# Performance work log

Measured on AMD Instinct MI355X. Metric: run time of the kernel, lower is better.

## Reference

```python
import jax, jax.numpy as jnp
import numpy as np

B, H, N, D, R, HIDDEN = 4, 12, 1025, 64, 1, 32


def _make_tables(N, R):
    # Geometry tables, mirroring FlexAttentionCPB.init_tables
    P = N - R
    S = int(P ** 0.5)
    assert S * S == P
    rng = np.arange(-(S - 1), S, dtype=np.float32)        # [2S-1]
    dY, dX = np.meshgrid(rng, rng, indexing='ij')
    rel = np.stack([dY / max(S - 1, 1), dX / max(S - 1, 1)], axis=-1).reshape(-1, 2)
    rel_table = np.sign(rel) * np.log1p(np.abs(rel))      # [(2S-1)^2, 2]
    yy = np.arange(S)
    Y, X = np.meshgrid(yy, yy, indexing='ij')
    flat = np.stack([Y, X], 0).reshape(2, -1)             # [2, P]
    d = (flat[:, :, None] - flat[:, None, :]).transpose(1, 2, 0).copy()  # [P,P,2]
    d[:, :, 0] += S - 1
    d[:, :, 1] += S - 1
    d[:, :, 0] *= 2 * S - 1
    l_idx = d.sum(-1).astype(np.int32)
    idx = np.full((N, N), -1, dtype=np.int32)
    idx[R:, R:] = l_idx
    return jnp.asarray(rel_table, jnp.float32), jnp.asarray(idx)


def setup_inputs() -> dict:
    key = jax.random.key(0)
    ks = jax.random.split(key, 8)
    rel_table, idx_table = _make_tables(N, R)
    return {
        'q': jax.random.normal(ks[0], (B, H, N, D), jnp.float32),
        'k': jax.random.normal(ks[1], (B, H, N, D), jnp.float32),
        'v': jax.random.normal(ks[2], (B, H, N, D), jnp.float32),
        'mu': jax.random.normal(ks[3], (B, H, 2, N), jnp.float32),
        'w1': jax.random.normal(ks[4], (2, HIDDEN), jnp.float32) * 0.5,
        'b1': jax.random.normal(ks[5], (HIDDEN,), jnp.float32) * 0.05,
        'w2': jax.random.normal(ks[6], (HIDDEN, H), jnp.float32) * 0.1,
        'gamma': jnp.zeros((H,), jnp.float32),   # nn.Parameter(torch.zeros(H))
        'rel_table': rel_table,
        'idx_table': idx_table,
    }


def reference(q, k, v, mu, w1, b1, w2, gamma, rel_table, idx_table):
    d = q.shape[-1]
    # CPB MLP: Linear(2,hidden)+GELU(exact)+Linear(hidden,H,no bias) -> [L,H]
    bt = jax.nn.gelu(rel_table @ w1 + b1, approximate=False) @ w2
    has_bias = (idx_table >= 0)                       # [N,N] == (q>=R)&(kv>=R)
    idx_c = jnp.where(has_bias, idx_table, 0)
    bias = jnp.transpose(bt[idx_c], (2, 0, 1))        # [H,N,N]
    mu_q = mu[:, :, 0, :]                             # [B,H,N]
    mu_k = mu[:, :, 1, :]
    gate = jax.nn.sigmoid(gamma)[None, :, None, None] * (
        mu_q[..., :, None] + mu_k[..., None, :])      # [B,H,N,N]
    scale = 1.0 / jnp.sqrt(jnp.asarray(d, q.dtype))
    scores = jnp.einsum('bhqd,bhkd->bhqk', q, k) * scale
    scores = scores + has_bias[None, None].astype(scores.dtype) * gate * bias[None]
    attn = jax.nn.softmax(scores, axis=-1)
    return jnp.einsum('bhqk,bhkd->bhqd', attn, v)
```

## Files before the change

kernel.cpp:

```cpp
#include <hip/hip_runtime.h>
#include <math.h>

#define B_ 4
#define H_ 12
#define N_ 1025
#define D_ 64
#define HID_ 32
#define TBL_ 3969
#define NQT 17
#define NBLK (B_ * H_ * NQT)
#define LOG2E 1.44269504f
#define THR_ 12.0f

typedef _Float16 half8 __attribute__((ext_vector_type(8)));
typedef __fp16 fp16x2 __attribute__((ext_vector_type(2)));
typedef float f32x4 __attribute__((ext_vector_type(4)));

#if defined(__has_builtin)
#if __has_builtin(__builtin_amdgcn_exp2f)
#define EX2 __builtin_amdgcn_exp2f
#else
#define EX2 exp2f
#endif
#else
#define EX2 exp2f
#endif

#define BTT_OFF 0
#define AKT_OFF 190512
#define KF_OFF 399408
#define VF_OFF 7084080

__device__ __forceinline__ void stage16(const _Float16* gsrc, _Float16* ldst) {
    __builtin_amdgcn_global_load_lds(
        (const __attribute__((address_space(1))) void*)gsrc,
        (__attribute__((address_space(3))) void*)ldst, 16, 0, 0);
}

__global__ __launch_bounds__(256) void prep(
    const float* __restrict__ K, const float* __restrict__ V,
    const float* __restrict__ MU, const float* __restrict__ GAMMA,
    const float* __restrict__ rel, const float* __restrict__ w1,
    const float* __restrict__ b1, const float* __restrict__ w2,
    _Float16* __restrict__ Kf, _Float16* __restrict__ Vf,
    float* __restrict__ akT, float* __restrict__ btT) {
    const int bid = blockIdx.x;
    const int tid = threadIdx.x;
    if (bid < NBLK) {
        __shared__ float Vls[64 * 65];
        const int bh = bid / NQT, kt = bid % NQT;
        const size_t base = (size_t)bh * (N_ * D_);
        const int k0 = kt * 64;
#pragma unroll
        for (int it = 0; it < 4; ++it) {
            const int idx = it * 256 + tid;
            const int kr = idx >> 4, c4 = (idx & 15) << 2;
            const int kg = k0 + kr;
            float4 v4 = make_float4(0, 0, 0, 0);
            if (kg < N_) v4 = *(const float4*)(V + base + (size_t)kg * D_ + c4);
            Vls[(c4 + 0) * 65 + kr] = v4.x;
            Vls[(c4 + 1) * 65 + kr] = v4.y;
            Vls[(c4 + 2) * 65 + kr] = v4.z;
            Vls[(c4 + 3) * 65 + kr] = v4.w;
        }
        __syncthreads();
        const int lane = tid & 63, lq = lane & 15, g = lane >> 4;
        const int fbh = tid >> 6;
        const size_t tb = (size_t)(bh * NQT + kt) * 4096;
#pragma unroll
        for (int x = 0; x < 2; ++x) {
            const int fb = fbh + x * 4;
            {
                const int kh = fb >> 2, dg = fb & 3;
                const float* vp = &Vls[(dg * 16 + lq) * 65 + kh * 32 + g * 8];
                half8 v8;
#pragma unroll
                for (int j = 0; j < 8; ++j) v8[j] = (_Float16)vp[j];
                *(half8*)&Vf[tb + fb * 512 + lane * 8] = v8;
            }
            {
                const int row = k0 + (fb >> 1) * 16 + lq;
                const int col = (fb & 1) * 32 + g * 8;
                half8 k8;
                if (row < N_) {
                    const float4* p = (const float4*)(K + base + (size_t)row * D_ + col);
                    float4 a = p[0], b = p[1];
                    k8[0] = (_Float16)a.x; k8[1] = (_Float16)a.y;
                    k8[2] = (_Float16)a.z; k8[3] = (_Float16)a.w;
                    k8[4] = (_Float16)b.x; k8[5] = (_Float16)b.y;
                    k8[6] = (_Float16)b.z; k8[7] = (_Float16)b.w;
                } else {
#pragma unroll
                    for (int j = 0; j < 8; ++j) k8[j] = (_Float16)0.f;
                }
                *(half8*)&Kf[tb + fb * 512 + lane * 8] = k8;
            }
        }
        if (tid < 64) {
            const int kk = k0 + tid;
            const int h = bh % H_;
            const float sgl = LOG2E / (1.f + __expf(-GAMMA[h]));
            float a = 0.f;
            if (kk >= 1 && kk < N_) a = sgl * MU[((size_t)bh * 2 + 1) * N_ + kk];
            akT[bh * 1088 + kk] = a;
        }
    } else {
        const int i = (bid - NBLK) * 256 + tid;
        if (i < TBL_) {
            const float x0 = rel[2 * i + 0], x1 = rel[2 * i + 1];
            float acc[H_];
#pragma unroll
            for (int h = 0; h < H_; ++h) acc[h] = 0.f;
#pragma unroll
            for (int j = 0; j < HID_; ++j) {
                float t = fmaf(x0, w1[j], fmaf(x1, w1[HID_ + j], b1[j]));
                float gl = 0.5f * t * (1.f + erff(t * 0.7071067811865475f));
#pragma unroll
                for (int h = 0; h < H_; ++h) acc[h] = fmaf(gl, w2[j * H_ + h], acc[h]);
            }
#pragma unroll
            for (int h = 0; h < H_; ++h) btT[h * TBL_ + i] = acc[h];
        }
    }
}

__global__ __launch_bounds__(256, 4) void flex_attn(
    const float* __restrict__ Q, const _Float16* __restrict__ Kf,
    const _Float16* __restrict__ Vf, const float* __restrict__ MU,
    const float* __restrict__ GAMMA, const char* __restrict__ btb,
    const float* __restrict__ akT, float* __restrict__ OUT) {
    __shared__ __align__(16) _Float16 Ks[2][4096];
    __shared__ __align__(16) _Float16 Vs[2][4096];
    __shared__ __align__(16) _Float16 Pl[4][1024];

    const int bid = blockIdx.x;
    const int swz0 = (bid & 7) * (NBLK / 8) + (bid >> 3);
    const int bh = swz0 / NQT;
    const int qt = swz0 % NQT;
    const int h = bh % H_;
    const int tid = threadIdx.x;
    const int w = tid >> 6;
    const int lane = tid & 63;
    const int lq = lane & 15;
    const int g = lane >> 4;

    const size_t base = (size_t)bh * (N_ * D_);
    const float sg = LOG2E / (1.f + __expf(-GAMMA[h]));

    const int qrow = qt * 64 + w * 16 + lq;
    const bool qv = qrow < N_;

    half8 qf[2];
#pragma unroll
    for (int dh = 0; dh < 2; ++dh) {
        float4 t0 = make_float4(0, 0, 0, 0), t1 = t0;
        if (qv) {
            const float4* qp = (const float4*)(Q + base + (size_t)qrow * D_ + dh * 32 + g * 8);
            t0 = qp[0]; t1 = qp[1];
        }
        const float qs = 0.125f * LOG2E;
        half8 q8;
        q8[0] = (_Float16)(t0.x * qs); q8[1] = (_Float16)(t0.y * qs);
        q8[2] = (_Float16)(t0.z * qs); q8[3] = (_Float16)(t0.w * qs);
        q8[4] = (_Float16)(t1.x * qs); q8[5] = (_Float16)(t1.y * qs);
        q8[6] = (_Float16)(t1.z * qs); q8[7] = (_Float16)(t1.w * qs);
        qf[dh] = q8;
    }

    const bool qb = qv && (qrow >= 1);
    const float qbf = qb ? 1.f : 0.f;
    float aq = 0.f;
    int cq = 0;
    if (qb) {
        const int pq = qrow - 1;
        cq = (pq >> 5) * 63 + (pq & 31);
        aq = sg * MU[(size_t)bh * 2 * N_ + qrow];
    }
    int boffs[16];
#pragma unroll
    for (int kg = 0; kg < 4; ++kg) {
#pragma unroll
        for (int r = 0; r < 4; ++r) {
            const int pk = kg * 16 + g * 4 + r - 1;
            const int ck = (pk >> 5) * 63 + (pk & 31);
            boffs[kg * 4 + r] = (h * TBL_ + cq + 1984 - ck) * 4 + 2048;
        }
    }
    const float* akb = akT + bh * 1088;
    const _Float16* kfb = Kf + (size_t)bh * NQT * 4096;
    const _Float16* vfb = Vf + (size_t)bh * NQT * 4096;

    f32x4 o[4];
    const f32x4 zz = {0.f, 0.f, 0.f, 0.f};
#pragma unroll
    for (int dg = 0; dg < 4; ++dg) o[dg] = zz;
    float m = 0.f, lsum = 0.f;

    stage16(kfb + (2 * w + 0) * 512 + lane * 8, &Ks[0][(2 * w + 0) * 512]);
    stage16(kfb + (2 * w + 1) * 512 + lane * 8, &Ks[0][(2 * w + 1) * 512]);
    stage16(vfb + (2 * w + 0) * 512 + lane * 8, &Vs[0][(2 * w + 0) * 512]);
    stage16(vfb + (2 * w + 1) * 512 + lane * 8, &Vs[0][(2 * w + 1) * 512]);
    __syncthreads();

    const int pswz = (lq & 7) << 4;
    char* plw = (char*)&Pl[w][0];

    for (int t = 0; t < NQT; ++t) {
        const int buf = t & 1;
        const int kt0 = t * 64;

        float bt16[16];
#pragma unroll
        for (int i = 0; i < 16; ++i) {
            int off = boffs[i];
            off = off < 2048 ? 2048 : off;
            bt16[i] = *(const float*)(btb + (uint32_t)off);
            boffs[i] -= 504;
        }
        f32x4 akq[4];
#pragma unroll
        for (int kg = 0; kg < 4; ++kg)
            akq[kg] = *(const f32x4*)(akb + kt0 + kg * 16 + g * 4);

        if (t + 1 < NQT) {
            const _Float16* kn = kfb + (size_t)(t + 1) * 4096;
            const _Float16* vn = vfb + (size_t)(t + 1) * 4096;
            stage16(kn + (2 * w + 0) * 512 + lane * 8, &Ks[buf ^ 1][(2 * w + 0) * 512]);
            stage16(kn + (2 * w + 1) * 512 + lane * 8, &Ks[buf ^ 1][(2 * w + 1) * 512]);
            stage16(vn + (2 * w + 0) * 512 + lane * 8, &Vs[buf ^ 1][(2 * w + 0) * 512]);
            stage16(vn + (2 * w + 1) * 512 + lane * 8, &Vs[buf ^ 1][(2 * w + 1) * 512]);
        }

        const _Float16* ksl = &Ks[buf][lane * 8];
        f32x4 sa[4];
#pragma unroll
        for (int kg = 0; kg < 4; ++kg) {
            half8 a0 = *(const half8*)(ksl + (2 * kg + 0) * 512);
            half8 a1 = *(const half8*)(ksl + (2 * kg + 1) * 512);
            f32x4 z = zz;
            z = __builtin_amdgcn_mfma_f32_16x16x32_f16(a0, qf[0], z, 0, 0, 0);
            z = __builtin_amdgcn_mfma_f32_16x16x32_f16(a1, qf[1], z, 0, 0, 0);
            sa[kg] = z;
        }

        if (t == 0 && g == 0) bt16[0] = 0.f;
        float s[16];
#pragma unroll
        for (int kg = 0; kg < 4; ++kg) {
#pragma unroll
            for (int r = 0; r < 4; ++r) {
                const int i = kg * 4 + r;
                s[i] = fmaf(fmaf(qbf, akq[kg][r], aq), bt16[i], sa[kg][r]);
            }
        }
        if (t == NQT - 1) {
#pragma unroll
            for (int kg = 0; kg < 4; ++kg)
#pragma unroll
                for (int r = 0; r < 4; ++r) {
                    const int i = kg * 4 + r;
                    if (1024 + kg * 16 + g * 4 + r >= N_) s[i] = -1e30f;
                }
        }

        float lmax = s[0];
#pragma unroll
        for (int i = 1; i < 16; ++i) lmax = fmaxf(lmax, s[i]);
        if (t == 0) {
            float mt = fmaxf(lmax, __shfl_xor(lmax, 16));
            m = fmaxf(mt, __shfl_xor(mt, 32));
        } else if (!__all(lmax <= m + THR_)) {
            float mt = fmaxf(lmax, __shfl_xor(lmax, 16));
            mt = fmaxf(mt, __shfl_xor(mt, 32));
            const float mnew = fmaxf(m, mt);
            const float cc = EX2(m - mnew);
            m = mnew;
            lsum *= cc;
            float cc4[4];
#pragma unroll
            for (int r = 0; r < 4; ++r) cc4[r] = __shfl(cc, g * 4 + r);
#pragma unroll
            for (int dg = 0; dg < 4; ++dg)
#pragma unroll
                for (int r = 0; r < 4; ++r) o[dg][r] *= cc4[r];
        }
        float pv16[16];
        float ls0 = 0.f, ls1 = 0.f;
#pragma unroll
        for (int i = 0; i < 16; i += 2) {
            pv16[i] = EX2(s[i] - m);
            pv16[i + 1] = EX2(s[i + 1] - m);
            ls0 += pv16[i];
            ls1 += pv16[i + 1];
        }
        lsum += ls0 + ls1;

#pragma unroll
        for (int kg = 0; kg < 4; ++kg) {
            fp16x2 h0 = __builtin_amdgcn_cvt_pkrtz(pv16[kg * 4 + 0], pv16[kg * 4 + 1]);
            fp16x2 h1 = __builtin_amdgcn_cvt_pkrtz(pv16[kg * 4 + 2], pv16[kg * 4 + 3]);
            uint2 u = make_uint2(__builtin_bit_cast(uint32_t, h0),
                                 __builtin_bit_cast(uint32_t, h1));
            *(uint2*)(plw + lq * 128 + ((kg * 32 + g * 8) ^ pswz)) = u;
        }

#pragma unroll
        for (int kh = 0; kh < 2; ++kh) {
            half8 pa = *(const half8*)(plw + lq * 128 + ((kh * 64 + g * 16) ^ pswz));
#pragma unroll
            for (int dg = 0; dg < 4; ++dg) {
                half8 vb8 = *(const half8*)&Vs[buf][(kh * 4 + dg) * 512 + lane * 8];
                o[dg] = __builtin_amdgcn_mfma_f32_16x16x32_f16(pa, vb8, o[dg], 0, 0, 0);
            }
        }
        __syncthreads();
    }

    lsum += __shfl_xor(lsum, 16);
    lsum += __shfl_xor(lsum, 32);
    const float linv = 1.f / lsum;
    float li4[4];
#pragma unroll
    for (int r = 0; r < 4; ++r) li4[r] = __shfl(linv, g * 4 + r);
#pragma unroll
    for (int dg = 0; dg < 4; ++dg) {
#pragma unroll
        for (int r = 0; r < 4; ++r) {
            const int qq = qt * 64 + w * 16 + g * 4 + r;
            if (qq < N_) OUT[base + (size_t)qq * D_ + dg * 16 + lq] = o[dg][r] * li4[r];
        }
    }
}

extern "C" void kernel_launch(void* const* d_in, const int* in_sizes, int n_in,
                              void* d_out, int out_size, void* d_ws, size_t ws_size,
                              hipStream_t stream) {
    const float* q = (const float*)d_in[0];
    const float* k = (const float*)d_in[1];
    const float* v = (const float*)d_in[2];
    const float* mu = (const float*)d_in[3];
    const float* w1 = (const float*)d_in[4];
    const float* b1 = (const float*)d_in[5];
    const float* w2 = (const float*)d_in[6];
    const float* gamma = (const float*)d_in[7];
    const float* rel = (const float*)d_in[8];

    char* ws = (char*)d_ws;
    float* btT = (float*)(ws + BTT_OFF);
    float* akT = (float*)(ws + AKT_OFF);
    _Float16* Kf = (_Float16*)(ws + KF_OFF);
    _Float16* Vf = (_Float16*)(ws + VF_OFF);

    prep<<<NBLK + (TBL_ + 255) / 256, 256, 0, stream>>>(k, v, mu, gamma, rel, w1, b1, w2,
                                                        Kf, Vf, akT, btT);
    flex_attn<<<NBLK, 256, 0, stream>>>(q, Kf, Vf, mu, gamma, ws - 2048, akT, (float*)d_out);
}
```

Before: 65.81 us.

## Switch attention to 32x32x16 MFMA with split-KV waves and register P

```diff
diff --git a/kernel.cpp b/kernel.cpp
--- a/kernel.cpp
+++ b/kernel.cpp
@@ -15,6 +15,7 @@
 typedef _Float16 half8 __attribute__((ext_vector_type(8)));
 typedef __fp16 fp16x2 __attribute__((ext_vector_type(2)));
 typedef float f32x4 __attribute__((ext_vector_type(4)));
+typedef float f32x16 __attribute__((ext_vector_type(16)));
 
 #if defined(__has_builtin)
 #if __has_builtin(__builtin_amdgcn_exp2f)
@@ -35,6 +36,11 @@
     __builtin_amdgcn_global_load_lds(
         (const __attribute__((address_space(1))) void*)gsrc,
         (__attribute__((address_space(3))) void*)ldst, 16, 0, 0);
+}
+
+__device__ __forceinline__ uint32_t pk2(float a, float b) {
+    fp16x2 t = __builtin_amdgcn_cvt_pkrtz(a, b);
+    return __builtin_bit_cast(uint32_t, t);
 }
 
 __global__ __launch_bounds__(256) void prep(
@@ -47,53 +53,59 @@
     const int bid = blockIdx.x;
     const int tid = threadIdx.x;
     if (bid < NBLK) {
-        __shared__ float Vls[64 * 65];
+        __shared__ uint32_t VlsU[64 * 36];
         const int bh = bid / NQT, kt = bid % NQT;
         const size_t base = (size_t)bh * (N_ * D_);
         const int k0 = kt * 64;
-#pragma unroll
-        for (int it = 0; it < 4; ++it) {
-            const int idx = it * 256 + tid;
-            const int kr = idx >> 4, c4 = (idx & 15) << 2;
-            const int kg = k0 + kr;
-            float4 v4 = make_float4(0, 0, 0, 0);
-            if (kg < N_) v4 = *(const float4*)(V + base + (size_t)kg * D_ + c4);
-            Vls[(c4 + 0) * 65 + kr] = v4.x;
-            Vls[(c4 + 1) * 65 + kr] = v4.y;
-            Vls[(c4 + 2) * 65 + kr] = v4.z;
-            Vls[(c4 + 3) * 65 + kr] = v4.w;
-        }
-        __syncthreads();
-        const int lane = tid & 63, lq = lane & 15, g = lane >> 4;
+        const int lane = tid & 63, q5 = lane & 31, hi = lane >> 5;
         const int fbh = tid >> 6;
         const size_t tb = (size_t)(bh * NQT + kt) * 4096;
+        float4 kld[2][2];
 #pragma unroll
         for (int x = 0; x < 2; ++x) {
-            const int fb = fbh + x * 4;
+            const int fk = fbh + 4 * x;
+            const int wk = fk >> 2, dc = fk & 3;
+            const int row = k0 + wk * 32 + q5;
+            const int col = dc * 16 + hi * 8;
+            kld[x][0] = make_float4(0, 0, 0, 0);
+            kld[x][1] = kld[x][0];
+            if (row < N_) {
+                const float4* p = (const float4*)(K + base + (size_t)row * D_ + col);
+                kld[x][0] = p[0];
+                kld[x][1] = p[1];
+            }
+        }
+#pragma unroll
+        for (int it = 0; it < 2; ++it) {
+            const int idx = it * 256 + tid;
+            const int p = idx >> 4;
+            const int c4 = (idx & 15) << 2;
+            const int r0 = k0 + 2 * p;
+            float4 a = make_float4(0, 0, 0, 0), b = a;
+            if (r0 < N_) a = *(const float4*)(V + base + (size_t)r0 * D_ + c4);
+            if (r0 + 1 < N_) b = *(const float4*)(V + base + (size_t)(r0 + 1) * D_ + c4);
+            VlsU[(c4 + 0) * 36 + p] = pk2(a.x, b.x);
+            VlsU[(c4 + 1) * 36 + p] = pk2(a.y, b.y);
+            VlsU[(c4 + 2) * 36 + p] = pk2(a.z, b.z);
+            VlsU[(c4 + 3) * 36 + p] = pk2(a.w, b.w);
+        }
+        __syncthreads();
+#pragma unroll
+        for (int x = 0; x < 2; ++x) {
+            const int f = fbh + 4 * x;
             {
-                const int kh = fb >> 2, dg = fb & 3;
-                const float* vp = &Vls[(dg * 16 + lq) * 65 + kh * 32 + g * 8];
-                half8 v8;
-#pragma unroll
-                for (int j = 0; j < 8; ++j) v8[j] = (_Float16)vp[j];
-                *(half8*)&Vf[tb + fb * 512 + lane * 8] = v8;
+                const int kc = f >> 1, dh = f & 1;
+                uint4 u = *(const uint4*)&VlsU[(dh * 32 + q5) * 36 + kc * 8 + hi * 4];
+                *(uint4*)&Vf[tb + f * 512 + lane * 8] = u;
             }
             {
-                const int row = k0 + (fb >> 1) * 16 + lq;
-                const int col = (fb & 1) * 32 + g * 8;
                 half8 k8;
-                if (row < N_) {
-                    const float4* p = (const float4*)(K + base + (size_t)row * D_ + col);
-                    float4 a = p[0], b = p[1];
-                    k8[0] = (_Float16)a.x; k8[1] = (_Float16)a.y;
-                    k8[2] = (_Float16)a.z; k8[3] = (_Float16)a.w;
-                    k8[4] = (_Float16)b.x; k8[5] = (_Float16)b.y;
-                    k8[6] = (_Float16)b.z; k8[7] = (_Float16)b.w;
-                } else {
-#pragma unroll
-                    for (int j = 0; j < 8; ++j) k8[j] = (_Float16)0.f;
-                }
-                *(half8*)&Kf[tb + fb * 512 + lane * 8] = k8;
+                float4 a = kld[x][0], b = kld[x][1];
+                k8[0] = (_Float16)a.x; k8[1] = (_Float16)a.y;
+                k8[2] = (_Float16)a.z; k8[3] = (_Float16)a.w;
+                k8[4] = (_Float16)b.x; k8[5] = (_Float16)b.y;
+                k8[6] = (_Float16)b.z; k8[7] = (_Float16)b.w;
+                *(half8*)&Kf[tb + f * 512 + lane * 8] = k8;
             }
         }
         if (tid < 64) {
@@ -124,14 +136,13 @@
     }
 }
 
-__global__ __launch_bounds__(256, 4) void flex_attn(
+__global__ __launch_bounds__(256, 3) void flex_attn(
     const float* __restrict__ Q, const _Float16* __restrict__ Kf,
     const _Float16* __restrict__ Vf, const float* __restrict__ MU,
     const float* __restrict__ GAMMA, const char* __restrict__ btb,
     const float* __restrict__ akT, float* __restrict__ OUT) {
     __shared__ __align__(16) _Float16 Ks[2][4096];
     __shared__ __align__(16) _Float16 Vs[2][4096];
-    __shared__ __align__(16) _Float16 Pl[4][1024];
 
     const int bid = blockIdx.x;
     const int swz0 = (bid & 7) * (NBLK / 8) + (bid >> 3);
@@ -140,31 +151,33 @@
     const int h = bh % H_;
     const int tid = threadIdx.x;
     const int w = tid >> 6;
+    const int wk = w & 1;
+    const int wq = w >> 1;
     const int lane = tid & 63;
-    const int lq = lane & 15;
-    const int g = lane >> 4;
+    const int q5 = lane & 31;
+    const int hi = lane >> 5;
 
     const size_t base = (size_t)bh * (N_ * D_);
     const float sg = LOG2E / (1.f + __expf(-GAMMA[h]));
 
-    const int qrow = qt * 64 + w * 16 + lq;
+    const int qrow = qt * 64 + wq * 32 + q5;
     const bool qv = qrow < N_;
 
-    half8 qf[2];
-#pragma unroll
-    for (int dh = 0; dh < 2; ++dh) {
+    half8 qf[4];
+    const float qs = 0.125f * LOG2E;
+#pragma unroll
+    for (int dc = 0; dc < 4; ++dc) {
         float4 t0 = make_float4(0, 0, 0, 0), t1 = t0;
         if (qv) {
-            const float4* qp = (const float4*)(Q + base + (size_t)qrow * D_ + dh * 32 + g * 8);
+            const float4* qp = (const float4*)(Q + base + (size_t)qrow * D_ + dc * 16 + hi * 8);
             t0 = qp[0]; t1 = qp[1];
         }
-        const float qs = 0.125f * LOG2E;
         half8 q8;
         q8[0] = (_Float16)(t0.x * qs); q8[1] = (_Float16)(t0.y * qs);
         q8[2] = (_Float16)(t0.z * qs); q8[3] = (_Float16)(t0.w * qs);
         q8[4] = (_Float16)(t1.x * qs); q8[5] = (_Float16)(t1.y * qs);
         q8[6] = (_Float16)(t1.z * qs); q8[7] = (_Float16)(t1.w * qs);
-        qf[dh] = q8;
+        qf[dc] = q8;
     }
 
     const bool qb = qv && (qrow >= 1);
@@ -178,23 +191,19 @@
     }
     int boffs[16];
 #pragma unroll
-    for (int kg = 0; kg < 4; ++kg) {
-#pragma unroll
-        for (int r = 0; r < 4; ++r) {
-            const int pk = kg * 16 + g * 4 + r - 1;
-            const int ck = (pk >> 5) * 63 + (pk & 31);
-            boffs[kg * 4 + r] = (h * TBL_ + cq + 1984 - ck) * 4 + 2048;
-        }
+    for (int r = 0; r < 16; ++r) {
+        const int pk = wk * 32 + (r & 3) + 8 * (r >> 2) + 4 * hi - 1;
+        const int ck = (pk >> 5) * 63 + (pk & 31);
+        boffs[r] = (h * TBL_ + cq + 1984 - ck) * 4 + 2048;
     }
     const float* akb = akT + bh * 1088;
     const _Float16* kfb = Kf + (size_t)bh * NQT * 4096;
     const _Float16* vfb = Vf + (size_t)bh * NQT * 4096;
 
-    f32x4 o[4];
-    const f32x4 zz = {0.f, 0.f, 0.f, 0.f};
-#pragma unroll
-    for (int dg = 0; dg < 4; ++dg) o[dg] = zz;
-    float m = 0.f, lsum = 0.f;
+    f32x16 oA, oB;
+#pragma unroll
+    for (int r = 0; r < 16; ++r) { oA[r] = 0.f; oB[r] = 0.f; }
+    float m = 0.f, l = 0.f;
 
     stage16(kfb + (2 * w + 0) * 512 + lane * 8, &Ks[0][(2 * w + 0) * 512]);
     stage16(kfb + (2 * w + 1) * 512 + lane * 8, &Ks[0][(2 * w + 1) * 512]);
@@ -202,25 +211,23 @@
     stage16(vfb + (2 * w + 1) * 512 + lane * 8, &Vs[0][(2 * w + 1) * 512]);
     __syncthreads();
 
-    const int pswz = (lq & 7) << 4;
-    char* plw = (char*)&Pl[w][0];
-
+#pragma unroll 1
     for (int t = 0; t < NQT; ++t) {
         const int buf = t & 1;
         const int kt0 = t * 64;
 
         float bt16[16];
 #pragma unroll
-        for (int i = 0; i < 16; ++i) {
-            int off = boffs[i];
+        for (int r = 0; r < 16; ++r) {
+            int off = boffs[r];
             off = off < 2048 ? 2048 : off;
-            bt16[i] = *(const float*)(btb + (uint32_t)off);
-            boffs[i] -= 504;
+            bt16[r] = *(const float*)(btb + (uint32_t)off);
+            boffs[r] -= 504;
         }
         f32x4 akq[4];
 #pragma unroll
-        for (int kg = 0; kg < 4; ++kg)
-            akq[kg] = *(const f32x4*)(akb + kt0 + kg * 16 + g * 4);
+        for (int mi = 0; mi < 4; ++mi)
+            akq[mi] = *(const f32x4*)(akb + kt0 + wk * 32 + 8 * mi + 4 * hi);
 
         if (t + 1 < NQT) {
             const _Float16* kn = kfb + (size_t)(t + 1) * 4096;
@@ -231,103 +238,122 @@
             stage16(vn + (2 * w + 1) * 512 + lane * 8, &Vs[buf ^ 1][(2 * w + 1) * 512]);
         }
 
-        const _Float16* ksl = &Ks[buf][lane * 8];
-        f32x4 sa[4];
-#pragma unroll
-        for (int kg = 0; kg < 4; ++kg) {
-            half8 a0 = *(const half8*)(ksl + (2 * kg + 0) * 512);
-            half8 a1 = *(const half8*)(ksl + (2 * kg + 1) * 512);
-            f32x4 z = zz;
-            z = __builtin_amdgcn_mfma_f32_16x16x32_f16(a0, qf[0], z, 0, 0, 0);
-            z = __builtin_amdgcn_mfma_f32_16x16x32_f16(a1, qf[1], z, 0, 0, 0);
-            sa[kg] = z;
-        }
-
-        if (t == 0 && g == 0) bt16[0] = 0.f;
+        const _Float16* ksl = &Ks[buf][wk * 2048 + lane * 8];
+        f32x16 sa;
+#pragma unroll
+        for (int r = 0; r < 16; ++r) sa[r] = 0.f;
+#pragma unroll
+        for (int dc = 0; dc < 4; ++dc) {
+            half8 a = *(const half8*)(ksl + dc * 512);
+            sa = __builtin_amdgcn_mfma_f32_32x32x16_f16(a, qf[dc], sa, 0, 0, 0);
+        }
+
+        if (t == 0 && wk == 0) bt16[0] = hi ? bt16[0] : 0.f;
         float s[16];
 #pragma unroll
-        for (int kg = 0; kg < 4; ++kg) {
-#pragma unroll
-            for (int r = 0; r < 4; ++r) {
-                const int i = kg * 4 + r;
-                s[i] = fmaf(fmaf(qbf, akq[kg][r], aq), bt16[i], sa[kg][r]);
-            }
-        }
+        for (int r = 0; r < 16; ++r)
+            s[r] = fmaf(fmaf(qbf, akq[r >> 2][r & 3], aq), bt16[r], sa[r]);
         if (t == NQT - 1) {
 #pragma unroll
-            for (int kg = 0; kg < 4; ++kg)
-#pragma unroll
-                for (int r = 0; r < 4; ++r) {
-                    const int i = kg * 4 + r;
-                    if (1024 + kg * 16 + g * 4 + r >= N_) s[i] = -1e30f;
-                }
-        }
-
-        float lmax = s[0];
-#pragma unroll
-        for (int i = 1; i < 16; ++i) lmax = fmaxf(lmax, s[i]);
+            for (int r = 0; r < 16; ++r) {
+                const bool keep = (wk == 0) && (r == 0) && (hi == 0);
+                s[r] = keep ? s[r] : -1e30f;
+            }
+        }
+
+        float mt = s[0];
+#pragma unroll
+        for (int r = 1; r < 16; ++r) mt = fmaxf(mt, s[r]);
         if (t == 0) {
-            float mt = fmaxf(lmax, __shfl_xor(lmax, 16));
             m = fmaxf(mt, __shfl_xor(mt, 32));
-        } else if (!__all(lmax <= m + THR_)) {
-            float mt = fmaxf(lmax, __shfl_xor(lmax, 16));
-            mt = fmaxf(mt, __shfl_xor(mt, 32));
-            const float mnew = fmaxf(m, mt);
+        } else if (!__all(mt <= m + THR_)) {
+            const float mp = fmaxf(mt, __shfl_xor(mt, 32));
+            const float mnew = fmaxf(m, mp);
             const float cc = EX2(m - mnew);
             m = mnew;
-            lsum *= cc;
-            float cc4[4];
-#pragma unroll
-            for (int r = 0; r < 4; ++r) cc4[r] = __shfl(cc, g * 4 + r);
-#pragma unroll
-            for (int dg = 0; dg < 4; ++dg)
-#pragma unroll
-                for (int r = 0; r < 4; ++r) o[dg][r] *= cc4[r];
+            l *= cc;
+#pragma unroll
+            for (int r = 0; r < 16; ++r) {
+                const int qr = (r & 3) + 8 * (r >> 2) + 4 * hi;
+                const float ccr = __shfl(cc, qr);
+                oA[r] *= ccr;
+                oB[r] *= ccr;
+            }
         }
         float pv16[16];
         float ls0 = 0.f, ls1 = 0.f;
 #pragma unroll
-        for (int i = 0; i < 16; i += 2) {
-            pv16[i] = EX2(s[i] - m);
-            pv16[i + 1] = EX2(s[i + 1] - m);
-            ls0 += pv16[i];
-            ls1 += pv16[i + 1];
-        }
-        lsum += ls0 + ls1;
-
-#pragma unroll
-        for (int kg = 0; kg < 4; ++kg) {
-            fp16x2 h0 = __builtin_amdgcn_cvt_pkrtz(pv16[kg * 4 + 0], pv16[kg * 4 + 1]);
-            fp16x2 h1 = __builtin_amdgcn_cvt_pkrtz(pv16[kg * 4 + 2], pv16[kg * 4 + 3]);
-            uint2 u = make_uint2(__builtin_bit_cast(uint32_t, h0),
-                                 __builtin_bit_cast(uint32_t, h1));
-            *(uint2*)(plw + lq * 128 + ((kg * 32 + g * 8) ^ pswz)) = u;
-        }
-
-#pragma unroll
-        for (int kh = 0; kh < 2; ++kh) {
-            half8 pa = *(const half8*)(plw + lq * 128 + ((kh * 64 + g * 16) ^ pswz));
-#pragma unroll
-            for (int dg = 0; dg < 4; ++dg) {
-                half8 vb8 = *(const half8*)&Vs[buf][(kh * 4 + dg) * 512 + lane * 8];
-                o[dg] = __builtin_amdgcn_mfma_f32_16x16x32_f16(pa, vb8, o[dg], 0, 0, 0);
-            }
+        for (int r = 0; r < 16; r += 2) {
+            pv16[r] = EX2(s[r] - m);
+            pv16[r + 1] = EX2(s[r + 1] - m);
+            ls0 += pv16[r];
+            ls1 += pv16[r + 1];
+        }
+        l += ls0 + ls1;
+
+        uint32_t pk[8];
+#pragma unroll
+        for (int c = 0; c < 8; ++c) {
+            const int mi = c >> 1, n = c & 1;
+            pk[c] = pk2(pv16[4 * mi + 2 * n], pv16[4 * mi + 2 * n + 1]);
+        }
+        asm volatile("v_permlane32_swap_b32 %0, %1" : "+v"(pk[0]), "+v"(pk[2]));
+        asm volatile("v_permlane32_swap_b32 %0, %1" : "+v"(pk[1]), "+v"(pk[3]));
+        asm volatile("v_permlane32_swap_b32 %0, %1" : "+v"(pk[4]), "+v"(pk[6]));
+        asm volatile("v_permlane32_swap_b32 %0, %1" : "+v"(pk[5]), "+v"(pk[7]));
+        const half8 pa0 = __builtin_bit_cast(half8, make_uint4(pk[0], pk[1], pk[2], pk[3]));
+        const half8 pa1 = __builtin_bit_cast(half8, make_uint4(pk[4], pk[5], pk[6], pk[7]));
+
+        const _Float16* vsl = &Vs[buf][wk * 2048 + lane * 8];
+        {
+            half8 v0 = *(const half8*)(vsl + 0 * 512);
+            half8 v1 = *(const half8*)(vsl + 1 * 512);
+            half8 v2 = *(const half8*)(vsl + 2 * 512);
+            half8 v3 = *(const half8*)(vsl + 3 * 512);
+            oA = __builtin_amdgcn_mfma_f32_32x32x16_f16(pa0, v0, oA, 0, 0, 0);
+            oB = __builtin_amdgcn_mfma_f32_32x32x16_f16(pa0, v1, oB, 0, 0, 0);
+            oA = __builtin_amdgcn_mfma_f32_32x32x16_f16(pa1, v2, oA, 0, 0, 0);
+            oB = __builtin_amdgcn_mfma_f32_32x32x16_f16(pa1, v3, oB, 0, 0, 0);
         }
         __syncthreads();
     }
 
-    lsum += __shfl_xor(lsum, 16);
-    lsum += __shfl_xor(lsum, 32);
-    const float linv = 1.f / lsum;
-    float li4[4];
-#pragma unroll
-    for (int r = 0; r < 4; ++r) li4[r] = __shfl(linv, g * 4 + r);
-#pragma unroll
-    for (int dg = 0; dg < 4; ++dg) {
-#pragma unroll
-        for (int r = 0; r < 4; ++r) {
-            const int qq = qt * 64 + w * 16 + g * 4 + r;
-            if (qq < N_) OUT[base + (size_t)qq * D_ + dg * 16 + lq] = o[dg][r] * li4[r];
+    const float lq_ = l + __shfl_xor(l, 32);
+    float* oxch = (float*)&Ks[0][0];
+    float* mlx = (float*)&Vs[0][0];
+    if (wk == 1) {
+        float* ox = oxch + wq * 2048;
+#pragma unroll
+        for (int r = 0; r < 16; ++r) {
+            const int qr = (r & 3) + 8 * (r >> 2) + 4 * hi;
+            ox[qr * 64 + q5] = oA[r];
+            ox[qr * 64 + 32 + q5] = oB[r];
+        }
+        if (hi == 0) {
+            mlx[wq * 64 + q5] = m;
+            mlx[wq * 64 + 32 + q5] = lq_;
+        }
+    }
+    __syncthreads();
+    if (wk == 0) {
+        const float m1 = mlx[wq * 64 + q5];
+        const float l1 = mlx[wq * 64 + 32 + q5];
+        const float ms = fmaxf(m, m1);
+        const float c0 = EX2(m - ms), c1 = EX2(m1 - ms);
+        const float inv = 1.f / fmaf(lq_, c0, l1 * c1);
+        const float f0 = c0 * inv, f1 = c1 * inv;
+        const float* ox = oxch + wq * 2048;
+#pragma unroll
+        for (int r = 0; r < 16; ++r) {
+            const int qr = (r & 3) + 8 * (r >> 2) + 4 * hi;
+            const float f0r = __shfl(f0, qr);
+            const float f1r = __shfl(f1, qr);
+            const int qq = qt * 64 + wq * 32 + qr;
+            if (qq < N_) {
+                float* op = OUT + base + (size_t)qq * D_;
+                op[q5] = fmaf(f0r, oA[r], f1r * ox[qr * 64 + q5]);
+                op[32 + q5] = fmaf(f0r, oB[r], f1r * ox[qr * 64 + 32 + q5]);
+            }
         }
     }
 }
```

After: 77.02 us. 17.0% more time.

## Store CPB bias table reversed in fp16 and gather contiguous runs with vector loads

Applied to the files above, without the earlier changes.

```diff
diff --git a/kernel.cpp b/kernel.cpp
--- a/kernel.cpp
+++ b/kernel.cpp
@@ -26,12 +26,17 @@
 #define EX2 exp2f
 #endif
 
-#define BTT_OFF 0
-#define AKT_OFF 190512
-#define KF_OFF 399408
-#define VF_OFF 7084080
+#define AKT_OFF 0
+#define BTH_OFF 208896
+#define KF_OFF 304160
+#define VF_OFF 6988832
 
 __device__ __forceinline__ void stage16(const _Float16* gsrc, _Float16* ldst) {
+    __builtin_amdgcn_global_load_lds(
+        (const __attribute__((address_space(1))) void*)gsrc,
+        (__attribute__((address_space(3))) void*)ldst, 16, 0, 0);
+}
+__device__ __forceinline__ void stage16f(const float* gsrc, float* ldst) {
     __builtin_amdgcn_global_load_lds(
         (const __attribute__((address_space(1))) void*)gsrc,
         (__attribute__((address_space(3))) void*)ldst, 16, 0, 0);
@@ -43,56 +48,71 @@
     const float* __restrict__ rel, const float* __restrict__ w1,
     const float* __restrict__ b1, const float* __restrict__ w2,
     _Float16* __restrict__ Kf, _Float16* __restrict__ Vf,
-    float* __restrict__ akT, float* __restrict__ btT) {
+    float* __restrict__ akT, _Float16* __restrict__ btH) {
     const int bid = blockIdx.x;
     const int tid = threadIdx.x;
     if (bid < NBLK) {
-        __shared__ float Vls[64 * 65];
+        __shared__ __align__(16) float Vf32[4096];
         const int bh = bid / NQT, kt = bid % NQT;
         const size_t base = (size_t)bh * (N_ * D_);
         const int k0 = kt * 64;
-#pragma unroll
-        for (int it = 0; it < 4; ++it) {
-            const int idx = it * 256 + tid;
-            const int kr = idx >> 4, c4 = (idx & 15) << 2;
-            const int kg = k0 + kr;
-            float4 v4 = make_float4(0, 0, 0, 0);
-            if (kg < N_) v4 = *(const float4*)(V + base + (size_t)kg * D_ + c4);
-            Vls[(c4 + 0) * 65 + kr] = v4.x;
-            Vls[(c4 + 1) * 65 + kr] = v4.y;
-            Vls[(c4 + 2) * 65 + kr] = v4.z;
-            Vls[(c4 + 3) * 65 + kr] = v4.w;
-        }
-        __syncthreads();
         const int lane = tid & 63, lq = lane & 15, g = lane >> 4;
         const int fbh = tid >> 6;
         const size_t tb = (size_t)(bh * NQT + kt) * 4096;
+        const float* vtile = V + base + (size_t)k0 * D_;
+
+#pragma unroll
+        for (int c = 0; c < 4; ++c) {
+            const int chunk = fbh * 4 + c;
+            const int kk = chunk * 4 + (lane >> 4);
+            const int doff = ((lane & 15) << 2) ^ (((kk >> 3) & 1) << 4);
+            const float* s = vtile + kk * 64 + doff;
+            if (k0 + chunk * 4 >= N_) s = vtile - (size_t)k0 * D_ + lane * 4;
+            stage16f(s, &Vf32[chunk * 256]);
+        }
+        float4 kld[2][2];
+#pragma unroll
+        for (int x = 0; x < 2; ++x) {
+            const int fb = fbh + x * 4;
+            const int row = k0 + (fb >> 1) * 16 + lq;
+            const int col = (fb & 1) * 32 + g * 8;
+            kld[x][0] = make_float4(0, 0, 0, 0);
+            kld[x][1] = kld[x][0];
+            if (row < N_) {
+                const float4* p = (const float4*)(K + base + (size_t)row * D_ + col);
+                kld[x][0] = p[0];
+                kld[x][1] = p[1];
+            }
+        }
+        __syncthreads();
+        const bool tail = (k0 + 64 > N_);
 #pragma unroll
         for (int x = 0; x < 2; ++x) {
             const int fb = fbh + x * 4;
             {
                 const int kh = fb >> 2, dg = fb & 3;
-                const float* vp = &Vls[(dg * 16 + lq) * 65 + kh * 32 + g * 8];
+                const int dphys = (dg * 16 + lq) ^ ((g & 1) << 4);
+                const float* vp = &Vf32[(kh * 32 + g * 8) * 64 + dphys];
                 half8 v8;
-#pragma unroll
-                for (int j = 0; j < 8; ++j) v8[j] = (_Float16)vp[j];
+                if (tail) {
+#pragma unroll
+                    for (int j = 0; j < 8; ++j) {
+                        const int row = k0 + kh * 32 + g * 8 + j;
+                        v8[j] = (row < N_) ? (_Float16)vp[j * 64] : (_Float16)0.f;
+                    }
+                } else {
+#pragma unroll
+                    for (int j = 0; j < 8; ++j) v8[j] = (_Float16)vp[j * 64];
+                }
                 *(half8*)&Vf[tb + fb * 512 + lane * 8] = v8;
             }
             {
-                const int row = k0 + (fb >> 1) * 16 + lq;
-                const int col = (fb & 1) * 32 + g * 8;
                 half8 k8;
-                if (row < N_) {
-                    const float4* p = (const float4*)(K + base + (size_t)row * D_ + col);
-                    float4 a = p[0], b = p[1];
-                    k8[0] = (_Float16)a.x; k8[1] = (_Float16)a.y;
-                    k8[2] = (_Float16)a.z; k8[3] = (_Float16)a.w;
-                    k8[4] = (_Float16)b.x; k8[5] = (_Float16)b.y;
-                    k8[6] = (_Float16)b.z; k8[7] = (_Float16)b.w;
-                } else {
-#pragma unroll
-                    for (int j = 0; j < 8; ++j) k8[j] = (_Float16)0.f;
-                }
+                float4 a = kld[x][0], b = kld[x][1];
+                k8[0] = (_Float16)a.x; k8[1] = (_Float16)a.y;
+                k8[2] = (_Float16)a.z; k8[3] = (_Float16)a.w;
+                k8[4] = (_Float16)b.x; k8[5] = (_Float16)b.y;
+                k8[6] = (_Float16)b.z; k8[7] = (_Float16)b.w;
                 *(half8*)&Kf[tb + fb * 512 + lane * 8] = k8;
             }
         }
@@ -119,7 +139,7 @@
                 for (int h = 0; h < H_; ++h) acc[h] = fmaf(gl, w2[j * H_ + h], acc[h]);
             }
 #pragma unroll
-            for (int h = 0; h < H_; ++h) btT[h * TBL_ + i] = acc[h];
+            for (int h = 0; h < H_; ++h) btH[h * TBL_ + (TBL_ - 1 - i)] = (_Float16)acc[h];
         }
     }
 }
@@ -127,7 +147,7 @@
 __global__ __launch_bounds__(256, 4) void flex_attn(
     const float* __restrict__ Q, const _Float16* __restrict__ Kf,
     const _Float16* __restrict__ Vf, const float* __restrict__ MU,
-    const float* __restrict__ GAMMA, const char* __restrict__ btb,
+    const float* __restrict__ GAMMA, const _Float16* __restrict__ btH,
     const float* __restrict__ akT, float* __restrict__ OUT) {
     __shared__ __align__(16) _Float16 Ks[2][4096];
     __shared__ __align__(16) _Float16 Vs[2][4096];
@@ -176,15 +196,14 @@
         cq = (pq >> 5) * 63 + (pq & 31);
         aq = sg * MU[(size_t)bh * 2 * N_ + qrow];
     }
-    int boffs[16];
+    const _Float16* bth = btH + h * TBL_;
+    int yq[4], pp[4];
 #pragma unroll
     for (int kg = 0; kg < 4; ++kg) {
-#pragma unroll
-        for (int r = 0; r < 4; ++r) {
-            const int pk = kg * 16 + g * 4 + r - 1;
-            const int ck = (pk >> 5) * 63 + (pk & 31);
-            boffs[kg * 4 + r] = (h * TBL_ + cq + 1984 - ck) * 4 + 2048;
-        }
+        const int pk0 = kg * 16 + g * 4 - 1;
+        const int ck0 = (pk0 >> 5) * 63 + (pk0 & 31);
+        yq[kg] = 1984 - cq + ck0;
+        pp[kg] = yq[kg] & 1;
     }
     const float* akb = akT + bh * 1088;
     const _Float16* kfb = Kf + (size_t)bh * NQT * 4096;
@@ -211,11 +230,29 @@
 
         float bt16[16];
 #pragma unroll
-        for (int i = 0; i < 16; ++i) {
-            int off = boffs[i];
-            off = off < 2048 ? 2048 : off;
-            bt16[i] = *(const float*)(btb + (uint32_t)off);
-            boffs[i] -= 504;
+        for (int kg = 0; kg < 4; ++kg) {
+            const int y0 = yq[kg];
+            const bool crossL = ((kg & 1) == 0) && (g == 0);
+            const int runY = crossL ? (y0 + 32) : y0;
+            const int be = runY & ~1;
+            const uint3 ld = *(const uint3*)(bth + be);
+            const uint32_t wa = pp[kg] ? ((ld.x >> 16) | (ld.y << 16)) : ld.x;
+            const uint32_t wb = pp[kg] ? ((ld.y >> 16) | (ld.z << 16)) : ld.y;
+            const float f0 = (float)__builtin_bit_cast(_Float16, (unsigned short)(wa & 0xffffu));
+            const float f1 = (float)__builtin_bit_cast(_Float16, (unsigned short)(wa >> 16));
+            const float f2 = (float)__builtin_bit_cast(_Float16, (unsigned short)(wb & 0xffffu));
+            const float f3 = (float)__builtin_bit_cast(_Float16, (unsigned short)(wb >> 16));
+            if ((kg & 1) == 0) {
+                const float fs = (float)bth[y0];
+                bt16[kg * 4 + 0] = crossL ? fs : f0;
+                bt16[kg * 4 + 1] = crossL ? f0 : f1;
+                bt16[kg * 4 + 2] = crossL ? f1 : f2;
+                bt16[kg * 4 + 3] = crossL ? f2 : f3;
+            } else {
+                bt16[kg * 4 + 0] = f0; bt16[kg * 4 + 1] = f1;
+                bt16[kg * 4 + 2] = f2; bt16[kg * 4 + 3] = f3;
+            }
+            yq[kg] += 126;
         }
         f32x4 akq[4];
 #pragma unroll
@@ -346,12 +383,12 @@
     const float* rel = (const float*)d_in[8];
 
     char* ws = (char*)d_ws;
-    float* btT = (float*)(ws + BTT_OFF);
     float* akT = (float*)(ws + AKT_OFF);
+    _Float16* btH = (_Float16*)(ws + BTH_OFF);
     _Float16* Kf = (_Float16*)(ws + KF_OFF);
     _Float16* Vf = (_Float16*)(ws + VF_OFF);
 
     prep<<<NBLK + (TBL_ + 255) / 256, 256, 0, stream>>>(k, v, mu, gamma, rel, w1, b1, w2,
-                                                        Kf, Vf, akT, btT);
-    flex_attn<<<NBLK, 256, 0, stream>>>(q, Kf, Vf, mu, gamma, ws - 2048, akT, (float*)d_out);
-}
+                                                        Kf, Vf, akT, btH);
+    flex_attn<<<NBLK, 256, 0, stream>>>(q, Kf, Vf, mu, gamma, btH, akT, (float*)d_out);
+}
```

Result: slower. 71.14 us (+8.1%).
